# Kernel optimization log

Measured on AMD Instinct MI355X. Metric: run time of the kernel, lower is better.

Reference implementation:

```python
import jax, jax.numpy as jnp
import numpy as np

B, S, D = 8, 2048, 128

def setup_inputs() -> dict:
    key = jax.random.key(0)
    kq, kk, kv = jax.random.split(key, 3)
    return {
        "Q": jax.random.normal(kq, (B, S, D), dtype=jnp.float32),
        "K": jax.random.normal(kk, (B, S, D), dtype=jnp.float32),
        "V": jax.random.normal(kv, (B, S, D), dtype=jnp.float32),
    }

def reference(Q, K, V):
    dim = Q.shape[-1]
    scores = jnp.einsum('bqd,bkd->bqk', Q, K) / jnp.sqrt(jnp.float32(dim))
    seq_len = Q.shape[1]
    # causal mask: -inf above the diagonal (matches torch.triu(ones*-inf, diagonal=1))
    causal = jnp.triu(jnp.full((seq_len, seq_len), -jnp.inf, dtype=scores.dtype), k=1)
    scores = scores + causal
    weights = jax.nn.softmax(scores, axis=-1)
    context = jnp.einsum('bqk,bkd->bqd', weights, V)
    return context
```

## Files before the change

kernel.cpp:

```cpp
#include <hip/hip_runtime.h>

#define B_ 8
#define S_ 2048
#define D_ 128
#define NT_ 64
#define FRAG_ 512

typedef __attribute__((ext_vector_type(4))) float f32x4;
typedef __attribute__((ext_vector_type(16))) float f32x16;
typedef __attribute__((ext_vector_type(8))) short bf16x8;
typedef __attribute__((ext_vector_type(4))) unsigned u32x4;
typedef __attribute__((ext_vector_type(2))) unsigned uint32x2;

#define MF(a, b, c) __builtin_amdgcn_mfma_f32_32x32x16_bf16(a, b, c, 0, 0, 0)

__device__ __forceinline__ short f2bf(float f) {
  union { float f; unsigned u; } x; x.f = f;
  unsigned r = x.u + 0x7FFFu + ((x.u >> 16) & 1u);
  return (short)(r >> 16);
}

__device__ __forceinline__ float exp2_hw(float x) {
  float r;
  asm("v_exp_f32 %0, %1" : "=v"(r) : "v"(x));
  return r;
}

__device__ __forceinline__ unsigned cvt_pk_bf16(float lo, float hi) {
  unsigned r;
  asm("v_cvt_pk_bf16_f32 %0, %1, %2" : "=v"(r) : "v"(lo), "v"(hi));
  return r;
}

__device__ __forceinline__ void plswap(unsigned& a, unsigned& b, int hi) {
#if __has_builtin(__builtin_amdgcn_permlane32_swap)
  uint32x2 r = __builtin_amdgcn_permlane32_swap(a, b, false, false);
  a = r[0]; b = r[1];
#else
  unsigned pa = (unsigned)__shfl_xor((int)a, 32, 64);
  unsigned pb = (unsigned)__shfl_xor((int)b, 32, 64);
  unsigned na = hi ? pb : a;
  unsigned nb = hi ? b : pa;
  a = na; b = nb;
#endif
}

__device__ __forceinline__ f32x16 zero16() {
  f32x16 v = {0.f,0.f,0.f,0.f,0.f,0.f,0.f,0.f,0.f,0.f,0.f,0.f,0.f,0.f,0.f,0.f};
  return v;
}

__global__ __launch_bounds__(256) void prep_frag(
    const float* __restrict__ Q, const float* __restrict__ K,
    const float* __restrict__ V, short* __restrict__ Qf,
    short* __restrict__ Kf, short* __restrict__ Vf) {
  __shared__ short qt[32][136], kt[32][136], vt[32][136];
  const int b  = blockIdx.x & 7;
  const int st = blockIdx.x >> 3;
  const int t  = threadIdx.x;
  const int row = t >> 3, c0 = (t & 7) * 16;
  const size_t base = ((size_t)(b * S_ + st * 32 + row)) * D_ + c0;
  const float scq = 0.12751744553939605f;

  #pragma unroll
  for (int i = 0; i < 4; ++i) {
    f32x4 q = *(const f32x4*)(Q + base + i * 4);
    f32x4 k = *(const f32x4*)(K + base + i * 4);
    f32x4 v = *(const f32x4*)(V + base + i * 4);
    #pragma unroll
    for (int j = 0; j < 4; ++j) {
      qt[row][c0 + i * 4 + j] = f2bf(q[j] * scq);
      kt[row][c0 + i * 4 + j] = f2bf(k[j]);
      vt[row][c0 + i * 4 + j] = f2bf(v[j]);
    }
  }
  __syncthreads();

  const int l = t & 63, ln = l & 31, hi = l >> 5, w = t >> 6;
  const size_t gidx = (size_t)(b * NT_ + st) * 8;
  #pragma unroll
  for (int i = 0; i < 2; ++i) {
    const int m = w * 2 + i;
    bf16x8 qv = *(const bf16x8*)&qt[ln][m * 16 + hi * 8];
    bf16x8 kv = *(const bf16x8*)&kt[ln][m * 16 + hi * 8];
    *(bf16x8*)(Qf + (gidx + m) * FRAG_ + l * 8) = qv;
    *(bf16x8*)(Kf + (gidx + m) * FRAG_ + l * 8) = kv;
    const int d4 = m >> 1, h = m & 1;
    bf16x8 vv;
    #pragma unroll
    for (int j = 0; j < 8; ++j) vv[j] = vt[h * 16 + hi * 8 + j][d4 * 32 + ln];
    *(bf16x8*)(Vf + (gidx + m) * FRAG_ + l * 8) = vv;
  }
}

__global__ __launch_bounds__(512) void fattn_fwd(
    const short* __restrict__ Qf, const short* __restrict__ Kf,
    const short* __restrict__ Vf, float* __restrict__ Og) {
  const int idx  = blockIdx.x;
  const int i    = 31 - (idx >> 3);
  const int b    = idx & 7;
  const int tid  = threadIdx.x;
  const int w    = __builtin_amdgcn_readfirstlane(tid >> 6);
  const int sub  = w >> 2;
  const int kv   = w & 3;
  const int tt   = 2 * i + sub;
  const int lane = tid & 63;
  const int ln   = lane & 31;
  const int hi   = lane >> 5;
  const int lane8 = lane * 8;

  const short* Qfb = Qf + (size_t)b * (NT_ * 8 * FRAG_);
  const short* Kfb = Kf + (size_t)b * (NT_ * 8 * FRAG_);
  const short* Vfb = Vf + (size_t)b * (NT_ * 8 * FRAG_);
  float*       Ob  = Og + (size_t)b * S_ * D_;

  __shared__ float ldsO[4][4][32][33];
  __shared__ float lS[8][32], invLS[32];

  bf16x8 qb[8];
  {
    const short* qfp = Qfb + (size_t)tt * (8 * FRAG_);
    #pragma unroll
    for (int dt = 0; dt < 8; ++dt)
      qb[dt] = *(const bf16x8*)(qfp + dt * FRAG_ + lane8);
  }

  f32x16 o[4];
  #pragma unroll
  for (int q = 0; q < 4; ++q) o[q] = zero16();
  float l_part = 0.f;

  int s = kv;
  if (s <= tt) {
    bf16x8 kb[8];
    {
      const short* kfp = Kfb + (size_t)s * (8 * FRAG_);
      #pragma unroll
      for (int dt = 0; dt < 8; ++dt)
        kb[dt] = *(const bf16x8*)(kfp + dt * FRAG_ + lane8);
    }

    for (;;) {
      const short* vfp = Vfb + (size_t)s * (8 * FRAG_);
      bf16x8 va[8];
      #pragma unroll
      for (int m8 = 0; m8 < 8; ++m8)
        va[m8] = *(const bf16x8*)(vfp + m8 * FRAG_ + lane8);

      f32x16 sv = zero16();
      __builtin_amdgcn_s_setprio(1);
      #pragma unroll
      for (int dt = 0; dt < 8; ++dt) sv = MF(kb[dt], qb[dt], sv);
      __builtin_amdgcn_s_setprio(0);

      const bool lastst = (s + 4 > tt);
      if (!lastst) {
        const short* k2 = Kfb + (size_t)(s + 4) * (8 * FRAG_);
        #pragma unroll
        for (int dt = 0; dt < 8; ++dt)
          kb[dt] = *(const bf16x8*)(k2 + dt * FRAG_ + lane8);
      }

      if (s == tt) {
        #pragma unroll
        for (int r = 0; r < 16; ++r) {
          const int kl = (r & 3) + 8 * (r >> 2) + 4 * hi;
          if (kl > ln) sv[r] = -512.0f;
        }
      }

      float p[16];
      #pragma unroll
      for (int r = 0; r < 16; ++r) p[r] = exp2_hw(sv[r]);
      float ts[8];
      #pragma unroll
      for (int r = 0; r < 8; ++r) ts[r] = p[r] + p[r + 8];
      #pragma unroll
      for (int r = 0; r < 4; ++r) ts[r] = ts[r] + ts[r + 4];
      l_part += (ts[0] + ts[1]) + (ts[2] + ts[3]);

      unsigned x0 = cvt_pk_bf16(p[0], p[1]),  x1 = cvt_pk_bf16(p[2], p[3]);
      unsigned y0 = cvt_pk_bf16(p[4], p[5]),  y1 = cvt_pk_bf16(p[6], p[7]);
      plswap(x0, y0, hi); plswap(x1, y1, hi);
      unsigned z0 = cvt_pk_bf16(p[8], p[9]),  z1 = cvt_pk_bf16(p[10], p[11]);
      unsigned w0 = cvt_pk_bf16(p[12], p[13]), w1 = cvt_pk_bf16(p[14], p[15]);
      plswap(z0, w0, hi); plswap(z1, w1, hi);
      u32x4 t0 = {x0, x1, y0, y1};
      u32x4 t1 = {z0, z1, w0, w1};
      bf16x8 pb0 = __builtin_bit_cast(bf16x8, t0);
      bf16x8 pb1 = __builtin_bit_cast(bf16x8, t1);

      __builtin_amdgcn_s_setprio(1);
      #pragma unroll
      for (int d4 = 0; d4 < 4; ++d4) {
        o[d4] = MF(va[d4 * 2],     pb0, o[d4]);
        o[d4] = MF(va[d4 * 2 + 1], pb1, o[d4]);
      }
      __builtin_amdgcn_s_setprio(0);

      if (lastst) break;
      s += 4;
    }
  }

  float l2 = l_part + __shfl_xor(l_part, 32, 64);
  if (hi == 0) lS[w][ln] = l2;

#define WRITE_O()                                                        \
  do {                                                                   \
    _Pragma("unroll")                                                    \
    for (int d4 = 0; d4 < 4; ++d4)                                       \
      _Pragma("unroll")                                                  \
      for (int r = 0; r < 16; ++r)                                       \
        ldsO[kv][d4][ln][(r & 3) + 8 * (r >> 2) + 4 * hi] = o[d4][r];    \
  } while (0)

#define MERGE_WRITE(q0_)                                                 \
  do {                                                                   \
    _Pragma("unroll")                                                    \
    for (int k = 0; k < 8; ++k) {                                        \
      const int e = k * 512 + tid;                                       \
      const int row = e >> 7;                                            \
      const int col = e & 127;                                           \
      float acc = ldsO[0][col >> 5][row][col & 31]                       \
                + ldsO[1][col >> 5][row][col & 31]                       \
                + ldsO[2][col >> 5][row][col & 31]                       \
                + ldsO[3][col >> 5][row][col & 31];                      \
      Ob[(size_t)((q0_) + row) * D_ + col] = acc * invLS[row];           \
    }                                                                    \
  } while (0)

  if (sub == 0) WRITE_O();
  __syncthreads();
  if (tid < 32)
    invLS[tid] = 1.0f / (lS[0][tid] + lS[1][tid] + lS[2][tid] + lS[3][tid]);
  __syncthreads();
  MERGE_WRITE(64 * i);
  __syncthreads();

  if (sub == 1) WRITE_O();
  __syncthreads();
  if (tid < 32)
    invLS[tid] = 1.0f / (lS[4][tid] + lS[5][tid] + lS[6][tid] + lS[7][tid]);
  __syncthreads();
  MERGE_WRITE(64 * i + 32);

#undef WRITE_O
#undef MERGE_WRITE
}

extern "C" void kernel_launch(void* const* d_in, const int* in_sizes, int n_in,
                              void* d_out, int out_size, void* d_ws, size_t ws_size,
                              hipStream_t stream) {
  const float* Q = (const float*)d_in[0];
  const float* K = (const float*)d_in[1];
  const float* V = (const float*)d_in[2];
  float* O = (float*)d_out;

  short* Qf = (short*)d_ws;
  short* Kf = Qf + (size_t)B_ * S_ * D_;
  short* Vf = Kf + (size_t)B_ * S_ * D_;

  prep_frag<<<B_ * NT_, 256, 0, stream>>>(Q, K, V, Qf, Kf, Vf);
  fattn_fwd<<<B_ * 32, 512, 0, stream>>>(Qf, Kf, Vf, O);
}
```

Before: 33.89 us.

## Stage K/V tiles into LDS via async DMA, double-buffered, with balanced tile pairing

```diff
diff --git a/kernel.cpp b/kernel.cpp
--- a/kernel.cpp
+++ b/kernel.cpp
@@ -50,6 +50,12 @@
   return v;
 }
 
+__device__ __forceinline__ void dma16(const short* g, short* l) {
+  __builtin_amdgcn_global_load_lds(
+      (const __attribute__((address_space(1))) void*)g,
+      (__attribute__((address_space(3))) void*)l, 16, 0, 0);
+}
+
 __global__ __launch_bounds__(256) void prep_frag(
     const float* __restrict__ Q, const float* __restrict__ K,
     const float* __restrict__ V, short* __restrict__ Qf,
@@ -68,10 +74,10 @@
     f32x4 k = *(const f32x4*)(K + base + i * 4);
     f32x4 v = *(const f32x4*)(V + base + i * 4);
     #pragma unroll
-    for (int j = 0; j < 4; ++j) {
-      qt[row][c0 + i * 4 + j] = f2bf(q[j] * scq);
-      kt[row][c0 + i * 4 + j] = f2bf(k[j]);
-      vt[row][c0 + i * 4 + j] = f2bf(v[j]);
+    for (int jj = 0; jj < 4; ++jj) {
+      qt[row][c0 + i * 4 + jj] = f2bf(q[jj] * scq);
+      kt[row][c0 + i * 4 + jj] = f2bf(k[jj]);
+      vt[row][c0 + i * 4 + jj] = f2bf(v[jj]);
     }
   }
   __syncthreads();
@@ -88,7 +94,7 @@
     const int d4 = m >> 1, h = m & 1;
     bf16x8 vv;
     #pragma unroll
-    for (int j = 0; j < 8; ++j) vv[j] = vt[h * 16 + hi * 8 + j][d4 * 32 + ln];
+    for (int jj = 0; jj < 8; ++jj) vv[jj] = vt[h * 16 + hi * 8 + jj][d4 * 32 + ln];
     *(bf16x8*)(Vf + (gidx + m) * FRAG_ + l * 8) = vv;
   }
 }
@@ -97,29 +103,44 @@
     const short* __restrict__ Qf, const short* __restrict__ Kf,
     const short* __restrict__ Vf, float* __restrict__ Og) {
   const int idx  = blockIdx.x;
-  const int i    = 31 - (idx >> 3);
+  const int j    = idx >> 3;
   const int b    = idx & 7;
   const int tid  = threadIdx.x;
   const int w    = __builtin_amdgcn_readfirstlane(tid >> 6);
   const int sub  = w >> 2;
-  const int kv   = w & 3;
-  const int tt   = 2 * i + sub;
+  const int par  = w & 3;
   const int lane = tid & 63;
   const int ln   = lane & 31;
   const int hi   = lane >> 5;
   const int lane8 = lane * 8;
+  const int my_tile = sub ? (63 - j) : j;
+  const int kmax = (67 - j) >> 2;
 
   const short* Qfb = Qf + (size_t)b * (NT_ * 8 * FRAG_);
   const short* Kfb = Kf + (size_t)b * (NT_ * 8 * FRAG_);
   const short* Vfb = Vf + (size_t)b * (NT_ * 8 * FRAG_);
   float*       Ob  = Og + (size_t)b * S_ * D_;
 
-  __shared__ float ldsO[4][4][32][33];
+  __shared__ __align__(16) char Sraw[131072];
+  short (*kvS)[4][8192] = (short (*)[4][8192])Sraw;
+  float (*ovl)[4][32][33] = (float (*)[4][32][33])Sraw;
   __shared__ float lS[8][32], invLS[32];
+
+#define STAGE(BUF, KK) do {                                              \
+    const int s_ = 4 * (KK) + (w >> 1);                                  \
+    if (s_ <= 63 - j) {                                                  \
+      const short* src_ = ((w & 1) ? Vfb : Kfb)                          \
+                          + (size_t)s_ * (8 * FRAG_) + lane8;            \
+      short* dst_ = &kvS[BUF][w >> 1][(w & 1) * 4096];                   \
+      _Pragma("unroll")                                                  \
+      for (int m_ = 0; m_ < 8; ++m_)                                     \
+        dma16(src_ + m_ * FRAG_, dst_ + m_ * 512);                       \
+    }                                                                    \
+  } while (0)
 
   bf16x8 qb[8];
   {
-    const short* qfp = Qfb + (size_t)tt * (8 * FRAG_);
+    const short* qfp = Qfb + (size_t)my_tile * (8 * FRAG_);
     #pragma unroll
     for (int dt = 0; dt < 8; ++dt)
       qb[dt] = *(const bf16x8*)(qfp + dt * FRAG_ + lane8);
@@ -127,41 +148,33 @@
 
   f32x16 o[4];
   #pragma unroll
-  for (int q = 0; q < 4; ++q) o[q] = zero16();
+  for (int i = 0; i < 4; ++i) o[i] = zero16();
   float l_part = 0.f;
 
-  int s = kv;
-  if (s <= tt) {
-    bf16x8 kb[8];
-    {
-      const short* kfp = Kfb + (size_t)s * (8 * FRAG_);
+  STAGE(0, 0);
+  asm volatile("s_waitcnt vmcnt(0)" ::: "memory");
+  __syncthreads();
+
+  #pragma unroll 1
+  for (int k = 0; k < kmax; ++k) {
+    const int buf = k & 1;
+    if (k + 1 < kmax) STAGE(buf ^ 1, k + 1);
+
+    const int s = 4 * k + par;
+    if (s <= my_tile) {
+      const short* ls = &kvS[buf][par][0];
+
+      bf16x8 kb[8];
       #pragma unroll
       for (int dt = 0; dt < 8; ++dt)
-        kb[dt] = *(const bf16x8*)(kfp + dt * FRAG_ + lane8);
-    }
-
-    for (;;) {
-      const short* vfp = Vfb + (size_t)s * (8 * FRAG_);
-      bf16x8 va[8];
-      #pragma unroll
-      for (int m8 = 0; m8 < 8; ++m8)
-        va[m8] = *(const bf16x8*)(vfp + m8 * FRAG_ + lane8);
-
+        kb[dt] = *(const bf16x8*)(ls + dt * 512 + lane8);
       f32x16 sv = zero16();
       __builtin_amdgcn_s_setprio(1);
       #pragma unroll
       for (int dt = 0; dt < 8; ++dt) sv = MF(kb[dt], qb[dt], sv);
       __builtin_amdgcn_s_setprio(0);
 
-      const bool lastst = (s + 4 > tt);
-      if (!lastst) {
-        const short* k2 = Kfb + (size_t)(s + 4) * (8 * FRAG_);
-        #pragma unroll
-        for (int dt = 0; dt < 8; ++dt)
-          kb[dt] = *(const bf16x8*)(k2 + dt * FRAG_ + lane8);
-      }
-
-      if (s == tt) {
+      if (s == my_tile) {
         #pragma unroll
         for (int r = 0; r < 16; ++r) {
           const int kl = (r & 3) + 8 * (r >> 2) + 4 * hi;
@@ -193,60 +206,57 @@
       __builtin_amdgcn_s_setprio(1);
       #pragma unroll
       for (int d4 = 0; d4 < 4; ++d4) {
-        o[d4] = MF(va[d4 * 2],     pb0, o[d4]);
-        o[d4] = MF(va[d4 * 2 + 1], pb1, o[d4]);
+        bf16x8 va0 = *(const bf16x8*)(ls + 4096 + (d4 * 2)     * 512 + lane8);
+        bf16x8 va1 = *(const bf16x8*)(ls + 4096 + (d4 * 2 + 1) * 512 + lane8);
+        o[d4] = MF(va0, pb0, o[d4]);
+        o[d4] = MF(va1, pb1, o[d4]);
       }
       __builtin_amdgcn_s_setprio(0);
-
-      if (lastst) break;
-      s += 4;
     }
+
+    asm volatile("s_waitcnt vmcnt(0)" ::: "memory");
+    __syncthreads();
   }
 
   float l2 = l_part + __shfl_xor(l_part, 32, 64);
   if (hi == 0) lS[w][ln] = l2;
-
-#define WRITE_O()                                                        \
-  do {                                                                   \
+  __syncthreads();
+
+#define MERGE_ROUND(SUBV, Q0) do {                                       \
+    if (sub == (SUBV)) {                                                 \
+      const int wv_ = w - (SUBV) * 4;                                    \
+      _Pragma("unroll")                                                  \
+      for (int d4 = 0; d4 < 4; ++d4)                                     \
+        _Pragma("unroll")                                                \
+        for (int r = 0; r < 16; ++r)                                     \
+          ovl[wv_][d4][ln][(r & 3) + 8 * (r >> 2) + 4 * hi] = o[d4][r];  \
+    }                                                                    \
+    __syncthreads();                                                     \
+    if (tid < 32) {                                                      \
+      const int base_ = (SUBV) * 4;                                      \
+      invLS[tid] = 1.0f / (lS[base_][tid] + lS[base_ + 1][tid] +         \
+                           lS[base_ + 2][tid] + lS[base_ + 3][tid]);     \
+    }                                                                    \
+    __syncthreads();                                                     \
     _Pragma("unroll")                                                    \
-    for (int d4 = 0; d4 < 4; ++d4)                                       \
-      _Pragma("unroll")                                                  \
-      for (int r = 0; r < 16; ++r)                                       \
-        ldsO[kv][d4][ln][(r & 3) + 8 * (r >> 2) + 4 * hi] = o[d4][r];    \
-  } while (0)
-
-#define MERGE_WRITE(q0_)                                                 \
-  do {                                                                   \
-    _Pragma("unroll")                                                    \
-    for (int k = 0; k < 8; ++k) {                                        \
-      const int e = k * 512 + tid;                                       \
+    for (int k2 = 0; k2 < 8; ++k2) {                                     \
+      const int e = k2 * 512 + tid;                                      \
       const int row = e >> 7;                                            \
       const int col = e & 127;                                           \
-      float acc = ldsO[0][col >> 5][row][col & 31]                       \
-                + ldsO[1][col >> 5][row][col & 31]                       \
-                + ldsO[2][col >> 5][row][col & 31]                       \
-                + ldsO[3][col >> 5][row][col & 31];                      \
-      Ob[(size_t)((q0_) + row) * D_ + col] = acc * invLS[row];           \
-    }                                                                    \
+      float acc = ovl[0][col >> 5][row][col & 31]                        \
+                + ovl[1][col >> 5][row][col & 31]                        \
+                + ovl[2][col >> 5][row][col & 31]                        \
+                + ovl[3][col >> 5][row][col & 31];                       \
+      Ob[(size_t)((Q0) + row) * D_ + col] = acc * invLS[row];            \
+    }                                                                    \
+    __syncthreads();                                                     \
   } while (0)
 
-  if (sub == 0) WRITE_O();
-  __syncthreads();
-  if (tid < 32)
-    invLS[tid] = 1.0f / (lS[0][tid] + lS[1][tid] + lS[2][tid] + lS[3][tid]);
-  __syncthreads();
-  MERGE_WRITE(64 * i);
-  __syncthreads();
-
-  if (sub == 1) WRITE_O();
-  __syncthreads();
-  if (tid < 32)
-    invLS[tid] = 1.0f / (lS[4][tid] + lS[5][tid] + lS[6][tid] + lS[7][tid]);
-  __syncthreads();
-  MERGE_WRITE(64 * i + 32);
-
-#undef WRITE_O
-#undef MERGE_WRITE
+  MERGE_ROUND(0, j * 32);
+  MERGE_ROUND(1, (63 - j) * 32);
+
+#undef MERGE_ROUND
+#undef STAGE
 }
 
 extern "C" void kernel_launch(void* const* d_in, const int* in_sizes, int n_in,
```

After: 38.34 us. +13.1%, slower.
